# Kernel tuning notes

Measured on AMD Instinct MI355X. Metric: run time of the kernel, lower is better.

Reference implementation:

```python
import jax, jax.numpy as jnp
import numpy as np
import math
from jax import lax

CANVAS = 300.0
NUM_CLASSES = 80
SCORE_THR = 0.01
K_CAND = 400   # candidates kept per image before NMS (cfg cltop=400)
K_OUT = 200    # final detections per image
IOU_THR = 0.45
CLIP = math.log(1000.0 / 16.0)  # exp clamp in decode_boxes
_FSIZES = [38, 19, 10, 5, 3, 1]
_STRIDES = [8, 16, 32, 64, 100, 300]
_SCALES = [0.07, 0.15, 0.33, 0.51, 0.69, 0.87, 1.05]
_AR3 = [1, 2, 3]
_ANUMS = [4, 6, 6, 6, 4, 4]


def _make_priors():
    # SSD300 priors (tv config: no rounding, clamp to canvas), cxcywh, [8732,4]
    out = []
    for i, (st, fs) in enumerate(zip(_STRIDES, _FSIZES)):
        s = _SCALES[i] * 300.0
        e = math.sqrt(_SCALES[i] * _SCALES[i + 1]) * 300.0
        ratios = [2.0, 0.5] + ([3.0, 1.0 / 3.0] if i in _AR3 else [])
        wh = [(s, s), (e, e)] + [(s * math.sqrt(r), s / math.sqrt(r)) for r in ratios]
        wh = np.array([(min(w, 300.0), min(h, 300.0)) for w, h in wh], np.float32)
        cy, cx = np.meshgrid(np.arange(fs), np.arange(fs), indexing='ij')
        ctr = np.stack([(cx + 0.5) * st, (cy + 0.5) * st], -1).reshape(-1, 2).astype(np.float32)
        A = wh.shape[0]
        out.append(np.concatenate([np.repeat(ctr, A, 0), np.tile(wh, (fs * fs, 1))], 1))
    return np.concatenate(out, 0)


def _head(x, w, b, tl):
    # Conv2d(c, an*tl, 3, 1, 1) -> permute(0,2,3,1) -> reshape(B, -1, tl)
    y = lax.conv_general_dilated(x, w, (1, 1), [(1, 1), (1, 1)],
                                 dimension_numbers=('NCHW', 'OIHW', 'NCHW'))
    y = y + b[None, :, None, None]
    n = y.shape[0]
    return jnp.transpose(y, (0, 2, 3, 1)).reshape(n, -1, tl)


def _decode(deltas, pri):
    cx = pri[:, 0] + deltas[:, 0] * 0.1 * pri[:, 2]
    cy = pri[:, 1] + deltas[:, 1] * 0.1 * pri[:, 3]
    w = pri[:, 2] * jnp.exp(jnp.minimum(deltas[:, 2] * 0.2, CLIP))
    h = pri[:, 3] * jnp.exp(jnp.minimum(deltas[:, 3] * 0.2, CLIP))
    b = jnp.stack([cx - 0.5 * w, cy - 0.5 * h, cx + 0.5 * w, cy + 0.5 * h], -1)
    return jnp.clip(b, 0.0, CANVAS)  # clamp_to_canvas


def _pairwise_iou(b):
    area = (b[:, 2] - b[:, 0]) * (b[:, 3] - b[:, 1])
    lt = jnp.maximum(b[:, None, :2], b[None, :, :2])
    rb = jnp.minimum(b[:, None, 2:], b[None, :, 2:])
    wh = jnp.clip(rb - lt, 0.0)
    inter = wh[..., 0] * wh[..., 1]
    return inter / (area[:, None] + area[None, :] - inter + 1e-9)


def _post_one(scr, reg, priors):
    # scr [A, C] (background already dropped), reg [A, 4]
    C = scr.shape[1]
    flat = jnp.where(scr > SCORE_THR, scr, 0.0).reshape(-1)
    s, idx = lax.top_k(flat, K_CAND)          # sorted desc -> greedy NMS order
    cls = idx % C + 1                          # bckg_class_first=False -> +1
    anc = idx // C
    boxes = _decode(reg[anc], priors[anc])
    valid = (s > 0.0) & (boxes[:, 2] > boxes[:, 0]) & (boxes[:, 3] > boxes[:, 1])
    s = jnp.where(valid, s, 0.0)
    # class-aware NMS via per-class coordinate offset (batched_nms trick)
    off = cls.astype(boxes.dtype)[:, None] * (CANVAS + 1.0)
    iou = _pairwise_iou(boxes + off)
    def body(i, keep):
        sup = (iou[i] > IOU_THR) & (jnp.arange(K_CAND) > i) & keep[i]
        return keep & (~sup)
    keep = lax.fori_loop(0, K_CAND, body, valid)
    fs, fi = lax.top_k(jnp.where(keep, s, 0.0), K_OUT)
    return boxes[fi], fs, jnp.where(fs > 0.0, cls[fi], 0).astype(jnp.int32)


def setup_inputs() -> dict:
    key = jax.random.key(0)
    shapes = [(16, 512, 38, 38), (16, 1024, 19, 19), (16, 512, 10, 10),
              (16, 256, 5, 5), (16, 256, 3, 3), (16, 256, 1, 1)]
    d = {}
    k = key
    for i, (shp, an) in enumerate(zip(shapes, _ANUMS)):
        c = shp[1]
        k, k1, k2, k3 = jax.random.split(k, 4)
        d['feat%d' % i] = jax.random.normal(k1, shp, jnp.float32)
        d['cls_w%d' % i] = jax.random.normal(k2, (an * (NUM_CLASSES + 1), c, 3, 3), jnp.float32) * 0.03
        d['cls_b%d' % i] = jnp.zeros((an * (NUM_CLASSES + 1),), jnp.float32)
        d['reg_w%d' % i] = jax.random.normal(k3, (an * 4, c, 3, 3), jnp.float32) * 0.03
        d['reg_b%d' % i] = jnp.zeros((an * 4,), jnp.float32)
    d['priors'] = jnp.asarray(_make_priors())
    return d


def reference(feat0, feat1, feat2, feat3, feat4, feat5,
              cls_w0, cls_b0, cls_w1, cls_b1, cls_w2, cls_b2,
              cls_w3, cls_b3, cls_w4, cls_b4, cls_w5, cls_b5,
              reg_w0, reg_b0, reg_w1, reg_b1, reg_w2, reg_b2,
              reg_w3, reg_b3, reg_w4, reg_b4, reg_w5, reg_b5,
              priors):
    feats = [feat0, feat1, feat2, feat3, feat4, feat5]
    cws = [cls_w0, cls_w1, cls_w2, cls_w3, cls_w4, cls_w5]
    cbs = [cls_b0, cls_b1, cls_b2, cls_b3, cls_b4, cls_b5]
    rws = [reg_w0, reg_w1, reg_w2, reg_w3, reg_w4, reg_w5]
    rbs = [reg_b0, reg_b1, reg_b2, reg_b3, reg_b4, reg_b5]
    cls = jnp.concatenate([_head(f, w, b, NUM_CLASSES + 1) for f, w, b in zip(feats, cws, cbs)], 1)
    reg = jnp.concatenate([_head(f, w, b, 4) for f, w, b in zip(feats, rws, rbs)], 1)
    scr = jax.nn.softmax(cls, axis=-1)[:, :, 1:]  # drop background (class 0)
    boxes, scores, classes = jax.vmap(_post_one, in_axes=(0, 0, None))(scr, reg, priors)
    return boxes, scores, classes
```

## Files before the change

### kernel.cpp

```cpp
#include <hip/hip_runtime.h>
#include <math.h>
#include <stdint.h>

#define NIMG 16
#define A_TOTAL 8732
#define NCLS 80
#define TL_CLS 81
#define CANVASF 300.0f
#define SCORE_THR 0.01f
#define IOU_THRF 0.45f
#define KCAND 400
#define KOUT 200
#define CAND_CAP 4096
#define NBIN 65536

typedef double d4 __attribute__((ext_vector_type(4)));

__device__ __forceinline__ float clampf(float v, float lo, float hi) {
    return fminf(fmaxf(v, lo), hi);
}

struct ConvJobs {
    const float* feat[6];
    const float* wgtT[6];
    const float* biasC[6];
    const float* biasR[6];
    float* outc;
    float* outr;
    int Cin[6], lgC[6], Hd[6], Mtot[6], Mcls[6], Mp[6], an[6], off[6];
    int nT[6], mW[6], jobTiles[6];
    int cum[8][7];
    int cs[8][6];
};

struct TransJobs {
    const float* srcC[6];
    const float* srcR[6];
    float* dst[6];
    int Cin[6], lgC[6], Mcls[6], Mtot[6], Mp[6], K[6], start[6];
    int total;
};

__global__ __launch_bounds__(256) void transpose_wgt(TransJobs tj)
{
    for (int idx = blockIdx.x * blockDim.x + threadIdx.x; idx < tj.total;
         idx += gridDim.x * blockDim.x) {
        int t = 0;
        while (t + 1 < 6 && idx >= tj.start[t + 1]) t++;
        int e = idx - tj.start[t];
        int k = e >> 9;
        int m = e & 511;
        if (m >= tj.Mp[t]) continue;
        int ci = k & (tj.Cin[t] - 1);
        int r = k >> tj.lgC[t];
        float v = 0.0f;
        if (m < tj.Mcls[t])
            v = tj.srcC[t][(size_t)m * tj.K[t] + (size_t)ci * 9 + r];
        else if (m < tj.Mtot[t])
            v = tj.srcR[t][(size_t)(m - tj.Mcls[t]) * tj.K[t] + (size_t)ci * 9 + r];
        tj.dst[t][(size_t)k * tj.Mp[t] + m] = v;
    }
}

__device__ __forceinline__ void conv_wave(
    const float* __restrict__ feat, const float* __restrict__ wgtT,
    const float* __restrict__ biasC, const float* __restrict__ biasR,
    float* __restrict__ outc, float* __restrict__ outr,
    int Cin, int lgC, int Hd, int Mtot, int Mcls, int Mp, int an, int lvl_off,
    int n0, int m0)
{
    const int K = Cin * 9;
    const int HW = Hd * Hd;
    const int N = NIMG * HW;
    const int CHW = Cin * HW;
    const int lane = threadIdx.x & 63;
    const int lm = lane & 15;
    const int lk = lane >> 4;

    int rowIdx[4], colIdx[4];
    {
        d4 z = (d4){0.0, 0.0, 0.0, 0.0};
        d4 pr = __builtin_amdgcn_mfma_f64_16x16x4f64((double)lm, 1.0, z, 0, 0, 0);
        d4 pc = __builtin_amdgcn_mfma_f64_16x16x4f64(1.0, (double)lm, z, 0, 0, 0);
#pragma unroll
        for (int i = 0; i < 4; i++) {
            rowIdx[i] = (int)(pr[i] * 0.25 + 0.5);
            colIdx[i] = (int)(pc[i] * 0.25 + 0.5);
        }
    }

    const int gPerR = Cin >> 2;
    const int KBg = K >> 2;

    int voffA = lk * Mp + m0 + lm;
    int voffB[4];
    float maskc[4];
    float bufA[2][2], bufB[2][4], bufM[2][4];

    d4 acc[2][4];
#pragma unroll
    for (int a = 0; a < 2; a++)
#pragma unroll
        for (int c = 0; c < 4; c++) acc[a][c] = (d4){0.0, 0.0, 0.0, 0.0};

    auto newR = [&](int r) {
        int ky = (r * 171) >> 9;
        int kx = r - 3 * ky;
#pragma unroll
        for (int c = 0; c < 4; c++) {
            int ng = n0 + lm + 16 * c;
            bool nv = ng < N;
            int bimg = 0, p = 0;
            if (nv) { bimg = ng / HW; p = ng - bimg * HW; }
            int y0 = p / Hd;
            int x0 = p - y0 * Hd;
            int yy = y0 + ky - 1;
            int xx = x0 + kx - 1;
            bool v = nv && (yy >= 0) && (yy < Hd) && (xx >= 0) && (xx < Hd);
            maskc[c] = v ? 1.0f : 0.0f;
            voffB[c] = bimg * CHW + lk * HW + (v ? (yy * Hd + xx) : 0);
        }
    };

    auto loadG = [&](int g, int slot) {
        if ((g & (gPerR - 1)) == 0) newR(g >> (lgC - 2));
#pragma unroll
        for (int c = 0; c < 4; c++) {
            bufB[slot][c] = feat[voffB[c]];
            bufM[slot][c] = maskc[c];
            voffB[c] += 4 * HW;
        }
        bufA[slot][0] = wgtT[voffA];
        bufA[slot][1] = wgtT[voffA + 16];
        voffA += 4 * Mp;
    };

    loadG(0, 0);
    loadG(1, 1);
    for (int g = 0; g < KBg; g += 2) {
        {
            double a0 = (double)bufA[0][0];
            double a1 = (double)bufA[0][1];
            double b0 = (double)(bufB[0][0] * bufM[0][0]);
            double b1 = (double)(bufB[0][1] * bufM[0][1]);
            double b2 = (double)(bufB[0][2] * bufM[0][2]);
            double b3 = (double)(bufB[0][3] * bufM[0][3]);
            if (g + 2 < KBg) loadG(g + 2, 0);
            acc[0][0] = __builtin_amdgcn_mfma_f64_16x16x4f64(a0, b0, acc[0][0], 0, 0, 0);
            acc[1][0] = __builtin_amdgcn_mfma_f64_16x16x4f64(a1, b0, acc[1][0], 0, 0, 0);
            acc[0][1] = __builtin_amdgcn_mfma_f64_16x16x4f64(a0, b1, acc[0][1], 0, 0, 0);
            acc[1][1] = __builtin_amdgcn_mfma_f64_16x16x4f64(a1, b1, acc[1][1], 0, 0, 0);
            acc[0][2] = __builtin_amdgcn_mfma_f64_16x16x4f64(a0, b2, acc[0][2], 0, 0, 0);
            acc[1][2] = __builtin_amdgcn_mfma_f64_16x16x4f64(a1, b2, acc[1][2], 0, 0, 0);
            acc[0][3] = __builtin_amdgcn_mfma_f64_16x16x4f64(a0, b3, acc[0][3], 0, 0, 0);
            acc[1][3] = __builtin_amdgcn_mfma_f64_16x16x4f64(a1, b3, acc[1][3], 0, 0, 0);
        }
        {
            double a0 = (double)bufA[1][0];
            double a1 = (double)bufA[1][1];
            double b0 = (double)(bufB[1][0] * bufM[1][0]);
            double b1 = (double)(bufB[1][1] * bufM[1][1]);
            double b2 = (double)(bufB[1][2] * bufM[1][2]);
            double b3 = (double)(bufB[1][3] * bufM[1][3]);
            if (g + 3 < KBg) loadG(g + 3, 1);
            acc[0][0] = __builtin_amdgcn_mfma_f64_16x16x4f64(a0, b0, acc[0][0], 0, 0, 0);
            acc[1][0] = __builtin_amdgcn_mfma_f64_16x16x4f64(a1, b0, acc[1][0], 0, 0, 0);
            acc[0][1] = __builtin_amdgcn_mfma_f64_16x16x4f64(a0, b1, acc[0][1], 0, 0, 0);
            acc[1][1] = __builtin_amdgcn_mfma_f64_16x16x4f64(a1, b1, acc[1][1], 0, 0, 0);
            acc[0][2] = __builtin_amdgcn_mfma_f64_16x16x4f64(a0, b2, acc[0][2], 0, 0, 0);
            acc[1][2] = __builtin_amdgcn_mfma_f64_16x16x4f64(a1, b2, acc[1][2], 0, 0, 0);
            acc[0][3] = __builtin_amdgcn_mfma_f64_16x16x4f64(a0, b3, acc[0][3], 0, 0, 0);
            acc[1][3] = __builtin_amdgcn_mfma_f64_16x16x4f64(a1, b3, acc[1][3], 0, 0, 0);
        }
    }

#pragma unroll
    for (int mi2 = 0; mi2 < 2; mi2++)
#pragma unroll
    for (int c = 0; c < 4; c++)
#pragma unroll
    for (int i = 0; i < 4; i++) {
        int mg = m0 + mi2 * 16 + rowIdx[i];
        int ng2 = n0 + c * 16 + colIdx[i];
        if (mg >= Mtot || ng2 >= N) continue;
        int b = ng2 / HW;
        int p = ng2 - b * HW;
        double val = acc[mi2][c][i];
        if (mg < Mcls) {
            int aidx = mg / TL_CLS;
            int t = mg - aidx * TL_CLS;
            int row = lvl_off + p * an + aidx;
            outc[((size_t)b * A_TOTAL + row) * TL_CLS + t] = (float)(val + (double)biasC[mg]);
        } else {
            int rm = mg - Mcls;
            int aidx = rm >> 2;
            int t = rm & 3;
            int row = lvl_off + p * an + aidx;
            outr[((size_t)b * A_TOTAL + row) * 4 + t] = (float)(val + (double)biasR[rm]);
        }
    }
}

__global__ __launch_bounds__(256, 4) void fused_conv(ConvJobs J)
{
    int bid = (int)blockIdx.x;
    int x = bid & 7;
    int r = bid >> 3;
    if (r >= J.cum[x][6]) return;
    int j = 0;
    while (j + 1 < 6 && r >= J.cum[x][j + 1]) j++;
    int blkInJob = J.cs[x][j] + (r - J.cum[x][j]);

    int wave = threadIdx.x >> 6;
    int tile = blkInJob * 4 + wave;
    if (tile >= J.jobTiles[j]) return;
    int mt = tile % J.mW[j];
    int nt = tile / J.mW[j];

    conv_wave(J.feat[j], J.wgtT[j], J.biasC[j], J.biasR[j], J.outc, J.outr,
              J.Cin[j], J.lgC[j], J.Hd[j], J.Mtot[j], J.Mcls[j], J.Mp[j],
              J.an[j], J.off[j], nt * 64, mt * 32);
}

__global__ __launch_bounds__(256) void softmax_kernel(
    const float* __restrict__ cls, float* __restrict__ scr, int nrows)
{
    __shared__ float buf[64 * 81];
    __shared__ float inv[64];
    const int row0 = blockIdx.x * 64;
    const int tid = threadIdx.x;

    for (int i = tid; i < 64 * 81; i += 256) {
        int r = row0 + i / 81;
        buf[i] = (r < nrows) ? cls[(size_t)row0 * 81 + i] : 0.0f;
    }
    __syncthreads();
    if (tid < 64) {
        float m = -1e30f;
        for (int c = 0; c < 81; c++) m = fmaxf(m, buf[tid * 81 + c]);
        double md = (double)m;
        double ssum = 0.0;
        for (int c = 0; c < 81; c++) {
            double e = exp((double)buf[tid * 81 + c] - md);
            buf[tid * 81 + c] = (float)e;
            ssum += e;
        }
        inv[tid] = (float)(1.0 / ssum);
    }
    __syncthreads();
    for (int i = tid; i < 64 * 80; i += 256) {
        int r = i / 80;
        int c = i - r * 80;
        int gr = row0 + r;
        if (gr < nrows) scr[(size_t)gr * 80 + c] = buf[r * 81 + c + 1] * inv[r];
    }
}

__global__ void zero_kernel(unsigned int* __restrict__ p, int n)
{
    int i = blockIdx.x * blockDim.x + threadIdx.x;
    if (i < n) p[i] = 0u;
}

__global__ void hist_kernel(const float* __restrict__ scr, unsigned int* __restrict__ hist)
{
    const int per_img = A_TOTAL * NCLS;
    const size_t total = (size_t)NIMG * per_img;
    for (size_t i = (size_t)blockIdx.x * blockDim.x + threadIdx.x; i < total;
         i += (size_t)gridDim.x * blockDim.x) {
        float v = scr[i];
        if (v > SCORE_THR) {
            int img = (int)(i / per_img);
            unsigned int u = __float_as_uint(v);
            atomicAdd(&hist[img * NBIN + (u >> 16)], 1u);
        }
    }
}

__global__ __launch_bounds__(1024) void select_kernel(
    const unsigned int* __restrict__ hist, unsigned int* __restrict__ sel)
{
    __shared__ unsigned int vals[1024];
    __shared__ unsigned int red[1024];
    __shared__ int s_total, s_b0, s_done;
    const int img = blockIdx.x;
    const int tid = threadIdx.x;
    if (tid == 0) { s_total = 0; s_b0 = 0; s_done = 0; }
    __syncthreads();
    for (int c = 63; c >= 0; c--) {
        unsigned int h = hist[img * NBIN + c * 1024 + tid];
        vals[tid] = h;
        red[tid] = h;
        __syncthreads();
        for (int s = 512; s > 0; s >>= 1) {
            if (tid < s) red[tid] += red[tid + s];
            __syncthreads();
        }
        if (tid == 0 && !s_done) {
            if (s_total + (int)red[0] >= KCAND) {
                int cum = s_total;
                for (int tt = 1023; tt >= 0; tt--) {
                    cum += (int)vals[tt];
                    if (cum >= KCAND) { s_b0 = c * 1024 + tt; s_done = 1; break; }
                }
            } else {
                s_total += (int)red[0];
            }
        }
        __syncthreads();
        if (s_done) break;
    }
    if (tid == 0) sel[img] = (unsigned int)s_b0;
}

__global__ void gather_kernel(const float* __restrict__ scr,
                              const unsigned int* __restrict__ sel,
                              unsigned int* __restrict__ candcnt,
                              uint2* __restrict__ cand)
{
    const int per_img = A_TOTAL * NCLS;
    const size_t total = (size_t)NIMG * per_img;
    for (size_t i = (size_t)blockIdx.x * blockDim.x + threadIdx.x; i < total;
         i += (size_t)gridDim.x * blockDim.x) {
        float v = scr[i];
        if (v > SCORE_THR) {
            int img = (int)(i / per_img);
            unsigned int u = __float_as_uint(v);
            if ((u >> 16) >= sel[img]) {
                unsigned int pos = atomicAdd(&candcnt[img], 1u);
                if (pos < CAND_CAP) {
                    unsigned int ridx = (unsigned int)(i - (size_t)img * per_img);
                    cand[(size_t)img * CAND_CAP + pos] = make_uint2(u, ridx);
                }
            }
        }
    }
}

__global__ __launch_bounds__(1024) void nms_kernel(
    const uint2* __restrict__ cand, const unsigned int* __restrict__ candcnt,
    const float* __restrict__ reg_all, const float* __restrict__ priors,
    float* __restrict__ out)
{
    __shared__ unsigned long long key[CAND_CAP];
    __shared__ float s_sc[KCAND];
    __shared__ float s_bx[KCAND][4];
    __shared__ float s_ob[KCAND][4];
    __shared__ float s_ar[KCAND];
    __shared__ float s_cl[KCAND];
    __shared__ int s_keep[KCAND];
    __shared__ int s_fi[KOUT];

    const int img = blockIdx.x;
    const int tid = threadIdx.x;
    unsigned int craw = candcnt[img];
    const int cnt = (craw > CAND_CAP) ? CAND_CAP : (int)craw;

    for (int i = tid; i < CAND_CAP; i += 1024) {
        unsigned long long kv = 0ull;
        if (i < cnt) {
            uint2 e = cand[(size_t)img * CAND_CAP + i];
            kv = ((unsigned long long)e.x << 32) | (unsigned int)(~e.y);
        }
        key[i] = kv;
    }
    __syncthreads();

    for (int ksz = 2; ksz <= CAND_CAP; ksz <<= 1) {
        for (int jj = ksz >> 1; jj > 0; jj >>= 1) {
            for (int i = tid; i < CAND_CAP; i += 1024) {
                int p = i ^ jj;
                if (p > i) {
                    bool desc = ((i & ksz) == 0);
                    unsigned long long a = key[i];
                    unsigned long long b = key[p];
                    bool sw = desc ? (a < b) : (a > b);
                    if (sw) { key[i] = b; key[p] = a; }
                }
            }
            __syncthreads();
        }
    }

    const float CLIPF = 4.135166556742356f;
    if (tid < KCAND) {
        const int j = tid;
        float s = 0.0f;
        unsigned int idx = 0u;
        if (j < cnt) {
            unsigned long long kv = key[j];
            unsigned int bits = (unsigned int)(kv >> 32);
            idx = ~((unsigned int)kv);
            s = __uint_as_float(bits);
        }
        int anc = (int)(idx / NCLS);
        int cl = (int)(idx - (unsigned int)anc * NCLS) + 1;
        const float* d = reg_all + ((size_t)img * A_TOTAL + anc) * 4;
        const float* pr = priors + (size_t)anc * 4;
        float d0 = d[0], d1 = d[1], d2 = d[2], d3 = d[3];
        float p0 = pr[0], p1 = pr[1], p2 = pr[2], p3 = pr[3];
        float cx = p0 + d0 * 0.1f * p2;
        float cy = p1 + d1 * 0.1f * p3;
        float t2 = fminf(d2 * 0.2f, CLIPF);
        float t3 = fminf(d3 * 0.2f, CLIPF);
        float bw = p2 * (float)exp((double)t2);
        float bh = p3 * (float)exp((double)t3);
        float x1 = clampf(cx - 0.5f * bw, 0.0f, CANVASF);
        float y1 = clampf(cy - 0.5f * bh, 0.0f, CANVASF);
        float x2 = clampf(cx + 0.5f * bw, 0.0f, CANVASF);
        float y2 = clampf(cy + 0.5f * bh, 0.0f, CANVASF);
        bool valid = (s > 0.0f) && (x2 > x1) && (y2 > y1);
        s = valid ? s : 0.0f;
        float off = (float)cl * (CANVASF + 1.0f);
        float ox1 = x1 + off, oy1 = y1 + off, ox2 = x2 + off, oy2 = y2 + off;
        s_sc[j] = s;
        s_cl[j] = (float)cl;
        s_keep[j] = valid ? 1 : 0;
        s_bx[j][0] = x1; s_bx[j][1] = y1; s_bx[j][2] = x2; s_bx[j][3] = y2;
        s_ob[j][0] = ox1; s_ob[j][1] = oy1; s_ob[j][2] = ox2; s_ob[j][3] = oy2;
        s_ar[j] = (ox2 - ox1) * (oy2 - oy1);
    }
    __syncthreads();

    for (int i = 0; i < KCAND; i++) {
        int ki = s_keep[i];
        if (ki && tid < KCAND && tid > i) {
            float lx = fmaxf(s_ob[i][0], s_ob[tid][0]);
            float ly = fmaxf(s_ob[i][1], s_ob[tid][1]);
            float rx = fminf(s_ob[i][2], s_ob[tid][2]);
            float ry = fminf(s_ob[i][3], s_ob[tid][3]);
            float iw = fmaxf(rx - lx, 0.0f);
            float ih = fmaxf(ry - ly, 0.0f);
            float inter = iw * ih;
            float iou = inter / (s_ar[i] + s_ar[tid] - inter + 1e-9f);
            if (iou > IOU_THRF) s_keep[tid] = 0;
        }
        __syncthreads();
    }

    if (tid == 0) {
        int pos = 0;
        for (int j = 0; j < KCAND && pos < KOUT; j++)
            if (s_keep[j]) s_fi[pos++] = j;
        for (int j = 0; j < KCAND && pos < KOUT; j++)
            if (!s_keep[j]) s_fi[pos++] = j;
    }
    __syncthreads();

    if (tid < KOUT) {
        int j = s_fi[tid];
        float fs = s_keep[j] ? s_sc[j] : 0.0f;
        size_t o = (size_t)img * KOUT + tid;
        out[o * 4 + 0] = s_bx[j][0];
        out[o * 4 + 1] = s_bx[j][1];
        out[o * 4 + 2] = s_bx[j][2];
        out[o * 4 + 3] = s_bx[j][3];
        out[(size_t)NIMG * KOUT * 4 + o] = fs;
        out[(size_t)NIMG * KOUT * 5 + o] = (fs > 0.0f) ? s_cl[j] : 0.0f;
    }
}

extern "C" void kernel_launch(void* const* d_in, const int* in_sizes, int n_in,
                              void* d_out, int out_size, void* d_ws, size_t ws_size,
                              hipStream_t stream)
{
    static const int Cin_[6] = {512, 1024, 512, 256, 256, 256};
    static const int lgC_[6] = {9, 10, 9, 8, 8, 8};
    static const int HW_[6]  = {38, 19, 10, 5, 3, 1};
    static const int an_[6]  = {4, 6, 6, 6, 4, 4};
    static const int off_[6] = {0, 5776, 7942, 8542, 8692, 8728};
    static const int Mp_[6]  = {352, 512, 512, 512, 352, 352};
    static const size_t wOffF_[6] = {0, 1622016, 6340608, 8699904, 0, 9879552};

    char* ws = (char*)d_ws;
    const size_t OFF_CLS  = 0;
    const size_t OFF_SCR  = 45266688;
    const size_t OFF_REG  = 89974528;
    const size_t OFF_HIST = 92209920;
    const size_t OFF_CCNT = 96404224;
    const size_t OFF_SEL  = 96404288;
    const size_t OFF_CAND = 96404352;

    float* cls_all = (float*)(ws + OFF_CLS);
    float* scr     = (float*)(ws + OFF_SCR);
    float* reg_all = (float*)(ws + OFF_REG);
    unsigned int* hist    = (unsigned int*)(ws + OFF_HIST);
    unsigned int* candcnt = (unsigned int*)(ws + OFF_CCNT);
    unsigned int* sel     = (unsigned int*)(ws + OFF_SEL);
    uint2* cand           = (uint2*)(ws + OFF_CAND);

    float* wT = scr;
    float* hT = (float*)hist;

    {
        TransJobs tj;
        int ts = 0;
        for (int L = 0; L < 6; L++) {
            tj.srcC[L] = (const float*)d_in[L * 5 + 1];
            tj.srcR[L] = (const float*)d_in[L * 5 + 3];
            tj.dst[L] = (L == 4) ? hT : (wT + wOffF_[L]);
            tj.Cin[L] = Cin_[L]; tj.lgC[L] = lgC_[L];
            tj.Mcls[L] = an_[L] * TL_CLS;
            tj.Mtot[L] = an_[L] * 85;
            tj.Mp[L] = Mp_[L];
            tj.K[L] = Cin_[L] * 9;
            tj.start[L] = ts; ts += Cin_[L] * 9 * 512;
        }
        tj.total = ts;
        transpose_wgt<<<4096, 256, 0, stream>>>(tj);
    }

    ConvJobs jobs;
    static const int ord_lvl[6] = {1, 0, 2, 3, 4, 5};
    int Bj[6];
    for (int q = 0; q < 6; q++) {
        int L = ord_lvl[q];
        int an = an_[L];
        jobs.feat[q]  = (const float*)d_in[L * 5 + 0];
        jobs.wgtT[q]  = (L == 4) ? hT : (wT + wOffF_[L]);
        jobs.biasC[q] = (const float*)d_in[L * 5 + 2];
        jobs.biasR[q] = (const float*)d_in[L * 5 + 4];
        jobs.Cin[q]   = Cin_[L];
        jobs.lgC[q]   = lgC_[L];
        jobs.Hd[q]    = HW_[L];
        jobs.Mcls[q]  = an * TL_CLS;
        jobs.Mtot[q]  = an * 85;
        jobs.Mp[q]    = Mp_[L];
        jobs.an[q]    = an;
        jobs.off[q]   = off_[L];
        int N = NIMG * HW_[L] * HW_[L];
        int nT = (N + 63) / 64;
        int mW = (jobs.Mtot[q] + 31) / 32;
        jobs.nT[q] = nT;
        jobs.mW[q] = mW;
        jobs.jobTiles[q] = nT * mW;
        Bj[q] = (nT * mW + 3) / 4;
    }
    int maxT = 0;
    for (int x = 0; x < 8; x++) {
        int acc = 0;
        for (int q = 0; q < 6; q++) {
            int s = (int)(((long long)x * Bj[q]) / 8);
            int e = (int)(((long long)(x + 1) * Bj[q]) / 8);
            jobs.cs[x][q] = s;
            jobs.cum[x][q] = acc;
            acc += e - s;
        }
        jobs.cum[x][6] = acc;
        if (acc > maxT) maxT = acc;
    }
    jobs.outc = cls_all;
    jobs.outr = reg_all;

    fused_conv<<<8 * maxT, 256, 0, stream>>>(jobs);

    {
        int nz = NIMG * NBIN + 16 + 16;
        zero_kernel<<<(nz + 255) / 256, 256, 0, stream>>>(hist, nz);
    }

    softmax_kernel<<<(NIMG * A_TOTAL + 63) / 64, 256, 0, stream>>>(cls_all, scr, NIMG * A_TOTAL);
    hist_kernel<<<2048, 256, 0, stream>>>(scr, hist);
    select_kernel<<<NIMG, 1024, 0, stream>>>(hist, sel);
    gather_kernel<<<2048, 256, 0, stream>>>(scr, sel, candcnt, cand);
    nms_kernel<<<NIMG, 1024, 0, stream>>>(cand, candcnt, reg_all,
                                          (const float*)d_in[30], (float*)d_out);
}
```

Before: 3.927 ms.

## Tile weight transpose through LDS and shrink conv N-tile for level 1

Replaces the grid-stride scalar weight transpose with a 32x32 LDS-tiled transpose that does float4 loads from the source and float4 stores to the destination. The conv wave is templated on the number of 16-column N subtiles, and level 1 uses 32-wide N tiles instead of 64 to create more tiles and better balance work across CUs. Smaller tiles reduce reuse of the A operand and add template code size. The new transpose assumes K and Mp are multiples of 32 and that source rows are float4-aligned.

```diff
diff --git a/kernel.cpp b/kernel.cpp
--- a/kernel.cpp
+++ b/kernel.cpp
@@ -27,8 +27,8 @@
     const float* biasR[6];
     float* outc;
     float* outr;
-    int Cin[6], lgC[6], Hd[6], Mtot[6], Mcls[6], Mp[6], an[6], off[6];
-    int nT[6], mW[6], jobTiles[6];
+    int Cin[6], lgC[6], Hd[6], Mtot[6], Mcls[6], Mp[6], an[6], off[6], cn[6];
+    int mW[6], jobTiles[6];
     int cum[8][7];
     int cs[8][6];
 };
@@ -37,31 +37,55 @@
     const float* srcC[6];
     const float* srcR[6];
     float* dst[6];
-    int Cin[6], lgC[6], Mcls[6], Mtot[6], Mp[6], K[6], start[6];
+    int Cin[6], K[6], Mcls[6], Mtot[6], Mp[6], mT[6], start[6];
     int total;
 };
 
 __global__ __launch_bounds__(256) void transpose_wgt(TransJobs tj)
 {
-    for (int idx = blockIdx.x * blockDim.x + threadIdx.x; idx < tj.total;
-         idx += gridDim.x * blockDim.x) {
-        int t = 0;
-        while (t + 1 < 6 && idx >= tj.start[t + 1]) t++;
-        int e = idx - tj.start[t];
-        int k = e >> 9;
-        int m = e & 511;
-        if (m >= tj.Mp[t]) continue;
-        int ci = k & (tj.Cin[t] - 1);
-        int r = k >> tj.lgC[t];
-        float v = 0.0f;
-        if (m < tj.Mcls[t])
-            v = tj.srcC[t][(size_t)m * tj.K[t] + (size_t)ci * 9 + r];
-        else if (m < tj.Mtot[t])
-            v = tj.srcR[t][(size_t)(m - tj.Mcls[t]) * tj.K[t] + (size_t)ci * 9 + r];
-        tj.dst[t][(size_t)k * tj.Mp[t] + m] = v;
-    }
-}
-
+    __shared__ float lds[32][33];
+    int bid = (int)blockIdx.x;
+    int L = 0;
+    while (L + 1 < 6 && bid >= tj.start[L + 1]) L++;
+    int rel = bid - tj.start[L];
+    int mTi = rel % tj.mT[L];
+    int kTi = rel / tj.mT[L];
+    int m0 = mTi * 32, k0 = kTi * 32;
+    const int K = tj.K[L];
+    const int tid = threadIdx.x;
+
+    {
+        int ml = tid >> 3;
+        int kq = (tid & 7) << 2;
+        int m = m0 + ml;
+        float4 v = make_float4(0.f, 0.f, 0.f, 0.f);
+        if (m < tj.Mcls[L])
+            v = *(const float4*)(tj.srcC[L] + (size_t)m * K + k0 + kq);
+        else if (m < tj.Mtot[L])
+            v = *(const float4*)(tj.srcR[L] + (size_t)(m - tj.Mcls[L]) * K + k0 + kq);
+        lds[kq + 0][ml] = v.x;
+        lds[kq + 1][ml] = v.y;
+        lds[kq + 2][ml] = v.z;
+        lds[kq + 3][ml] = v.w;
+    }
+    __syncthreads();
+    {
+        int kk = tid >> 3;
+        int mq = (tid & 7) << 2;
+        int k = k0 + kk;
+        int ci = k / 9;
+        int r = k - ci * 9;
+        int kp = r * tj.Cin[L] + ci;
+        float4 w;
+        w.x = lds[kk][mq + 0];
+        w.y = lds[kk][mq + 1];
+        w.z = lds[kk][mq + 2];
+        w.w = lds[kk][mq + 3];
+        *(float4*)(tj.dst[L] + (size_t)kp * tj.Mp[L] + m0 + mq) = w;
+    }
+}
+
+template<int CN>
 __device__ __forceinline__ void conv_wave(
     const float* __restrict__ feat, const float* __restrict__ wgtT,
     const float* __restrict__ biasC, const float* __restrict__ biasR,
@@ -93,21 +117,21 @@
     const int KBg = K >> 2;
 
     int voffA = lk * Mp + m0 + lm;
-    int voffB[4];
-    float maskc[4];
-    float bufA[2][2], bufB[2][4], bufM[2][4];
-
-    d4 acc[2][4];
+    int voffB[CN];
+    float maskc[CN];
+    float bufA[2][2], bufB[2][CN], bufM[2][CN];
+
+    d4 acc[2][CN];
 #pragma unroll
     for (int a = 0; a < 2; a++)
 #pragma unroll
-        for (int c = 0; c < 4; c++) acc[a][c] = (d4){0.0, 0.0, 0.0, 0.0};
+        for (int c = 0; c < CN; c++) acc[a][c] = (d4){0.0, 0.0, 0.0, 0.0};
 
     auto newR = [&](int r) {
         int ky = (r * 171) >> 9;
         int kx = r - 3 * ky;
 #pragma unroll
-        for (int c = 0; c < 4; c++) {
+        for (int c = 0; c < CN; c++) {
             int ng = n0 + lm + 16 * c;
             bool nv = ng < N;
             int bimg = 0, p = 0;
@@ -125,7 +149,7 @@
     auto loadG = [&](int g, int slot) {
         if ((g & (gPerR - 1)) == 0) newR(g >> (lgC - 2));
 #pragma unroll
-        for (int c = 0; c < 4; c++) {
+        for (int c = 0; c < CN; c++) {
             bufB[slot][c] = feat[voffB[c]];
             bufM[slot][c] = maskc[c];
             voffB[c] += 4 * HW;
@@ -141,43 +165,35 @@
         {
             double a0 = (double)bufA[0][0];
             double a1 = (double)bufA[0][1];
-            double b0 = (double)(bufB[0][0] * bufM[0][0]);
-            double b1 = (double)(bufB[0][1] * bufM[0][1]);
-            double b2 = (double)(bufB[0][2] * bufM[0][2]);
-            double b3 = (double)(bufB[0][3] * bufM[0][3]);
+            double bb[CN];
+#pragma unroll
+            for (int c = 0; c < CN; c++) bb[c] = (double)(bufB[0][c] * bufM[0][c]);
             if (g + 2 < KBg) loadG(g + 2, 0);
-            acc[0][0] = __builtin_amdgcn_mfma_f64_16x16x4f64(a0, b0, acc[0][0], 0, 0, 0);
-            acc[1][0] = __builtin_amdgcn_mfma_f64_16x16x4f64(a1, b0, acc[1][0], 0, 0, 0);
-            acc[0][1] = __builtin_amdgcn_mfma_f64_16x16x4f64(a0, b1, acc[0][1], 0, 0, 0);
-            acc[1][1] = __builtin_amdgcn_mfma_f64_16x16x4f64(a1, b1, acc[1][1], 0, 0, 0);
-            acc[0][2] = __builtin_amdgcn_mfma_f64_16x16x4f64(a0, b2, acc[0][2], 0, 0, 0);
-            acc[1][2] = __builtin_amdgcn_mfma_f64_16x16x4f64(a1, b2, acc[1][2], 0, 0, 0);
-            acc[0][3] = __builtin_amdgcn_mfma_f64_16x16x4f64(a0, b3, acc[0][3], 0, 0, 0);
-            acc[1][3] = __builtin_amdgcn_mfma_f64_16x16x4f64(a1, b3, acc[1][3], 0, 0, 0);
+#pragma unroll
+            for (int c = 0; c < CN; c++) {
+                acc[0][c] = __builtin_amdgcn_mfma_f64_16x16x4f64(a0, bb[c], acc[0][c], 0, 0, 0);
+                acc[1][c] = __builtin_amdgcn_mfma_f64_16x16x4f64(a1, bb[c], acc[1][c], 0, 0, 0);
+            }
         }
         {
             double a0 = (double)bufA[1][0];
             double a1 = (double)bufA[1][1];
-            double b0 = (double)(bufB[1][0] * bufM[1][0]);
-            double b1 = (double)(bufB[1][1] * bufM[1][1]);
-            double b2 = (double)(bufB[1][2] * bufM[1][2]);
-            double b3 = (double)(bufB[1][3] * bufM[1][3]);
+            double bb[CN];
+#pragma unroll
+            for (int c = 0; c < CN; c++) bb[c] = (double)(bufB[1][c] * bufM[1][c]);
             if (g + 3 < KBg) loadG(g + 3, 1);
-            acc[0][0] = __builtin_amdgcn_mfma_f64_16x16x4f64(a0, b0, acc[0][0], 0, 0, 0);
-            acc[1][0] = __builtin_amdgcn_mfma_f64_16x16x4f64(a1, b0, acc[1][0], 0, 0, 0);
-            acc[0][1] = __builtin_amdgcn_mfma_f64_16x16x4f64(a0, b1, acc[0][1], 0, 0, 0);
-            acc[1][1] = __builtin_amdgcn_mfma_f64_16x16x4f64(a1, b1, acc[1][1], 0, 0, 0);
-            acc[0][2] = __builtin_amdgcn_mfma_f64_16x16x4f64(a0, b2, acc[0][2], 0, 0, 0);
-            acc[1][2] = __builtin_amdgcn_mfma_f64_16x16x4f64(a1, b2, acc[1][2], 0, 0, 0);
-            acc[0][3] = __builtin_amdgcn_mfma_f64_16x16x4f64(a0, b3, acc[0][3], 0, 0, 0);
-            acc[1][3] = __builtin_amdgcn_mfma_f64_16x16x4f64(a1, b3, acc[1][3], 0, 0, 0);
+#pragma unroll
+            for (int c = 0; c < CN; c++) {
+                acc[0][c] = __builtin_amdgcn_mfma_f64_16x16x4f64(a0, bb[c], acc[0][c], 0, 0, 0);
+                acc[1][c] = __builtin_amdgcn_mfma_f64_16x16x4f64(a1, bb[c], acc[1][c], 0, 0, 0);
+            }
         }
     }
 
 #pragma unroll
     for (int mi2 = 0; mi2 < 2; mi2++)
 #pragma unroll
-    for (int c = 0; c < 4; c++)
+    for (int c = 0; c < CN; c++)
 #pragma unroll
     for (int i = 0; i < 4; i++) {
         int mg = m0 + mi2 * 16 + rowIdx[i];
@@ -217,9 +233,14 @@
     int mt = tile % J.mW[j];
     int nt = tile / J.mW[j];
 
-    conv_wave(J.feat[j], J.wgtT[j], J.biasC[j], J.biasR[j], J.outc, J.outr,
-              J.Cin[j], J.lgC[j], J.Hd[j], J.Mtot[j], J.Mcls[j], J.Mp[j],
-              J.an[j], J.off[j], nt * 64, mt * 32);
+    if (J.cn[j] == 2)
+        conv_wave<2>(J.feat[j], J.wgtT[j], J.biasC[j], J.biasR[j], J.outc, J.outr,
+                     J.Cin[j], J.lgC[j], J.Hd[j], J.Mtot[j], J.Mcls[j], J.Mp[j],
+                     J.an[j], J.off[j], nt * 32, mt * 32);
+    else
+        conv_wave<4>(J.feat[j], J.wgtT[j], J.biasC[j], J.biasR[j], J.outc, J.outr,
+                     J.Cin[j], J.lgC[j], J.Hd[j], J.Mtot[j], J.Mcls[j], J.Mp[j],
+                     J.an[j], J.off[j], nt * 64, mt * 32);
 }
 
 __global__ __launch_bounds__(256) void softmax_kernel(
@@ -499,15 +520,17 @@
             tj.srcC[L] = (const float*)d_in[L * 5 + 1];
             tj.srcR[L] = (const float*)d_in[L * 5 + 3];
             tj.dst[L] = (L == 4) ? hT : (wT + wOffF_[L]);
-            tj.Cin[L] = Cin_[L]; tj.lgC[L] = lgC_[L];
+            tj.Cin[L] = Cin_[L];
+            tj.K[L] = Cin_[L] * 9;
             tj.Mcls[L] = an_[L] * TL_CLS;
             tj.Mtot[L] = an_[L] * 85;
             tj.Mp[L] = Mp_[L];
-            tj.K[L] = Cin_[L] * 9;
-            tj.start[L] = ts; ts += Cin_[L] * 9 * 512;
+            tj.mT[L] = Mp_[L] / 32;
+            tj.start[L] = ts;
+            ts += (Mp_[L] / 32) * (Cin_[L] * 9 / 32);
         }
         tj.total = ts;
-        transpose_wgt<<<4096, 256, 0, stream>>>(tj);
+        transpose_wgt<<<ts, 256, 0, stream>>>(tj);
     }
 
     ConvJobs jobs;
@@ -528,10 +551,11 @@
         jobs.Mp[q]    = Mp_[L];
         jobs.an[q]    = an;
         jobs.off[q]   = off_[L];
+        jobs.cn[q]    = (L == 1) ? 2 : 4;
         int N = NIMG * HW_[L] * HW_[L];
-        int nT = (N + 63) / 64;
+        int nstep = 16 * jobs.cn[q];
+        int nT = (N + nstep - 1) / nstep;
         int mW = (jobs.Mtot[q] + 31) / 32;
-        jobs.nT[q] = nT;
         jobs.mW[q] = mW;
         jobs.jobTiles[q] = nT * mW;
         Bj[q] = (nT * mW + 3) / 4;
```

After: 3.769 ms. 4.0% less time.
